# Kernel optimization log

Measured on AMD Instinct MI355X. Metric: run time of the kernel, lower is better.

The kernel has to match this reference:

```python
import jax, jax.numpy as jnp
import numpy as np

HIDDEN = 1024
N_HEADS = 16
HEAD_DIM = HIDDEN // N_HEADS


def setup_inputs() -> dict:
    key = jax.random.key(0)
    ks = jax.random.split(key, 8)
    bs, seq = 8, 1024
    hidden_states = jax.random.normal(ks[0], (bs, seq, HIDDEN), dtype=jnp.float32)
    attention_mask = jnp.zeros((bs, 1, 1, seq), dtype=jnp.float32)
    s = 1.0 / np.sqrt(HIDDEN)
    Wq = jax.random.normal(ks[1], (HIDDEN, HIDDEN), dtype=jnp.float32) * s
    bq = jnp.zeros((HIDDEN,), dtype=jnp.float32)
    Wk = jax.random.normal(ks[2], (HIDDEN, HIDDEN), dtype=jnp.float32) * s
    bk = jnp.zeros((HIDDEN,), dtype=jnp.float32)
    Wv = jax.random.normal(ks[3], (HIDDEN, HIDDEN), dtype=jnp.float32) * s
    bv = jnp.zeros((HIDDEN,), dtype=jnp.float32)
    return {"hidden_states": hidden_states, "attention_mask": attention_mask,
            "Wq": Wq, "bq": bq, "Wk": Wk, "bk": bk, "Wv": Wv, "bv": bv}


def _split_heads(x):
    # [b, s, H] -> [b, h, s, d]
    b, s, _ = x.shape
    return x.reshape(b, s, N_HEADS, HEAD_DIM).transpose(0, 2, 1, 3)


def reference(hidden_states, attention_mask, Wq, bq, Wk, bk, Wv, bv):
    q = _split_heads(hidden_states @ Wq.T + bq)
    k = _split_heads(hidden_states @ Wk.T + bk)
    v = _split_heads(hidden_states @ Wv.T + bv)
    scale = 1.0 / np.sqrt(HEAD_DIM).astype(np.float32)
    scores = jnp.einsum('bhqd,bhkd->bhqk', q, k) * scale + attention_mask
    probs = jax.nn.softmax(scores, axis=-1)  # dropout p=0.0 -> identity
    ctx = jnp.einsum('bhqk,bhkd->bhqd', probs, v)
    b, h, s, d = ctx.shape
    return ctx.transpose(0, 2, 1, 3).reshape(b, s, h * d)
```

## Files before the change

### kernel.cpp

```cpp
#include <hip/hip_runtime.h>
#include <stdint.h>
#include <stddef.h>

#define HIDDEN 1024
#define NHEADS 16
#define HDIM   64
#define BS     8
#define SEQ    1024
#define MTOT   (BS*SEQ)
#define QKV_T  ((size_t)MTOT*HIDDEN)

typedef short    bf16x8 __attribute__((ext_vector_type(8)));
typedef short    bf16x4 __attribute__((ext_vector_type(4)));
typedef float    f32x4  __attribute__((ext_vector_type(4)));
typedef uint16_t u16x4  __attribute__((ext_vector_type(4)));

__device__ __forceinline__ uint16_t f2bf(float f) {
  union { float f; uint32_t u; } c; c.f = f;
  uint32_t u = c.u + 0x7FFFu + ((c.u >> 16) & 1u);
  return (uint16_t)(u >> 16);
}

__device__ __forceinline__ uint32_t cvt_pk_bf16(float lo, float hi) {
  uint32_t r;
  asm("v_cvt_pk_bf16_f32 %0, %1, %2" : "=v"(r) : "v"(lo), "v"(hi));
  return r;
}

__device__ __forceinline__ bf16x4 pack_bf16x4(float a, float b, float c, float d) {
  union { uint2 u; bf16x4 v; } cv;
  cv.u.x = cvt_pk_bf16(a, b);
  cv.u.y = cvt_pk_bf16(c, d);
  return cv.v;
}

__device__ __forceinline__ f32x4 mfma_16x16x16(bf16x4 a, bf16x4 b, f32x4 c) {
#if __has_builtin(__builtin_amdgcn_mfma_f32_16x16x16bf16_1k)
  return __builtin_amdgcn_mfma_f32_16x16x16bf16_1k(a, b, c, 0, 0, 0);
#elif __has_builtin(__builtin_amdgcn_mfma_f32_16x16x16_bf16)
  return __builtin_amdgcn_mfma_f32_16x16x16_bf16(a, b, c, 0, 0, 0);
#else
  f32x4 d;
  asm("v_mfma_f32_16x16x16_bf16 %0, %1, %2, %3"
      : "=&v"(d) : "v"(a), "v"(b), "v"(c));
  return d;
#endif
}

__device__ __forceinline__ float exp2fast(float x) {
#if __has_builtin(__builtin_amdgcn_exp2f)
  return __builtin_amdgcn_exp2f(x);
#else
  return __expf(x * 0.69314718056f);
#endif
}

__device__ __forceinline__ void gload_lds16(const uint16_t* g, uint16_t* lds) {
  __builtin_amdgcn_global_load_lds(
      (const __attribute__((address_space(1))) uint32_t*)g,
      (__attribute__((address_space(3))) uint32_t*)lds, 16, 0, 0);
}

__global__ __launch_bounds__(256) void cvt_kernel(
    const float* __restrict__ hs, const float* __restrict__ wq,
    const float* __restrict__ wk, const float* __restrict__ wv,
    uint16_t* __restrict__ hsb, uint16_t* __restrict__ wcat)
{
  const int i4 = blockIdx.x * 256 + threadIdx.x;
  f32x4 v;
  u16x4 o;
  if (i4 < 2097152) {
    v = *((const f32x4*)hs + i4);
    o[0]=f2bf(v[0]); o[1]=f2bf(v[1]); o[2]=f2bf(v[2]); o[3]=f2bf(v[3]);
    *((u16x4*)hsb + i4) = o;
  } else {
    int j4 = i4 - 2097152;
    int w  = j4 >> 18;
    int r4 = j4 & 262143;
    const float* src = (w == 0) ? wq : ((w == 1) ? wk : wv);
    v = *((const f32x4*)src + r4);
    o[0]=f2bf(v[0]); o[1]=f2bf(v[1]); o[2]=f2bf(v[2]); o[3]=f2bf(v[3]);
    *((u16x4*)wcat + j4) = o;
  }
}

__global__ __launch_bounds__(512, 4) void gemm_qkv(
    const uint16_t* __restrict__ hsb, const uint16_t* __restrict__ wcat,
    const float* __restrict__ bq, const float* __restrict__ bk,
    const float* __restrict__ bv, uint16_t* __restrict__ qbuf,
    uint16_t* __restrict__ kbuf, uint16_t* __restrict__ vtbuf)
{
  __shared__ uint16_t Alds[2][256*32];
  __shared__ uint16_t Blds[2][128*32];

  const int bid = blockIdx.x;
  const int wg  = (bid & 7) * 96 + (bid >> 3);
  const int tm  = wg / 24, tn = wg % 24;
  const int m0  = tm * 256, n0 = tn * 128;
  const int t   = threadIdx.x;
  const int l   = t & 63, w = t >> 6;
  const int wm  = w >> 1, wn = w & 1;
  const int q16 = l & 15;

  f32x4 acc[4][4];
#pragma unroll
  for (int i = 0; i < 4; i++)
#pragma unroll
    for (int j = 0; j < 4; j++) acc[i][j] = (f32x4){0.f,0.f,0.f,0.f};

  const int lrow = l >> 2;
  const int rB   = w * 16 + lrow;
  const int gsw  = (l & 3) ^ ((rB >> 1) & 3);
  const size_t offA0 = (size_t)rB * HIDDEN + gsw * 8;
  const size_t offA1 = (size_t)(128 + rB) * HIDDEN + gsw * 8;
  const size_t offB  = offA0;

  auto STAGE = [&](int buf, int kt) {
    const uint16_t* Ab = hsb  + (size_t)m0 * HIDDEN + kt * 32;
    const uint16_t* Bb = wcat + (size_t)n0 * HIDDEN + kt * 32;
    gload_lds16(Ab + offA0, &Alds[buf][(w * 16) * 32]);
    gload_lds16(Ab + offA1, &Alds[buf][(128 + w * 16) * 32]);
    gload_lds16(Bb + offB,  &Blds[buf][(w * 16) * 32]);
  };

  auto COMPUTE = [&](int buf) {
    bf16x8 af[4], bfr[4];
    const int G = l >> 4;
#pragma unroll
    for (int i = 0; i < 4; i++) {
      int ar = wm * 64 + i * 16 + q16;
      int gs = (G ^ ((ar >> 1) & 3)) & 3;
      af[i] = *(const bf16x8*)&Alds[buf][ar * 32 + gs * 8];
    }
#pragma unroll
    for (int j = 0; j < 4; j++) {
      int br = wn * 64 + j * 16 + q16;
      int gs = (G ^ ((br >> 1) & 3)) & 3;
      bfr[j] = *(const bf16x8*)&Blds[buf][br * 32 + gs * 8];
    }
    __builtin_amdgcn_s_setprio(1);
#pragma unroll
    for (int i = 0; i < 4; i++)
#pragma unroll
      for (int j = 0; j < 4; j++)
        acc[i][j] = __builtin_amdgcn_mfma_f32_16x16x32_bf16(af[i], bfr[j], acc[i][j], 0, 0, 0);
    __builtin_amdgcn_s_setprio(0);
  };

  STAGE(0, 0);
  STAGE(1, 1);
#pragma unroll 1
  for (int kt = 0; kt < 32; ++kt) {
    if (kt < 31) { asm volatile("s_waitcnt vmcnt(3)" ::: "memory"); }
    else         { asm volatile("s_waitcnt vmcnt(0)" ::: "memory"); }
    __builtin_amdgcn_s_barrier();
    __builtin_amdgcn_sched_barrier(0);
    COMPUTE(kt & 1);
    if (kt < 31) {
      __builtin_amdgcn_s_barrier();
      __builtin_amdgcn_sched_barrier(0);
      if (kt < 30) STAGE(kt & 1, kt + 2);
    }
  }

#pragma unroll
  for (int j = 0; j < 4; j++) {
    int n     = n0 + wn * 64 + j * 16 + q16;
    int which = n >> 10, nn = n & 1023;
    const float* bp = (which == 0) ? bq : ((which == 1) ? bk : bv);
    float bias = bp[nn];
    int hh = nn >> 6, dd = nn & 63;
#pragma unroll
    for (int i = 0; i < 4; i++) {
      if (which == 2) {
        int m_  = m0 + wm * 64 + i * 16 + (l >> 4) * 4;
        int b_  = m_ >> 10, s_ = m_ & 1023;
        size_t bhh = (size_t)(b_ * NHEADS + hh);
        uint2 pk;
        pk.x = cvt_pk_bf16(acc[i][j][0] + bias, acc[i][j][1] + bias);
        pk.y = cvt_pk_bf16(acc[i][j][2] + bias, acc[i][j][3] + bias);
        *(uint2*)&vtbuf[(bhh * HDIM + dd) * SEQ + s_] = pk;
      } else {
#pragma unroll
        for (int r = 0; r < 4; r++) {
          int m  = m0 + wm * 64 + i * 16 + (l >> 4) * 4 + r;
          int b_ = m >> 10, s_ = m & 1023;
          float val = acc[i][j][r] + bias;
          size_t bhh = (size_t)(b_ * NHEADS + hh);
          if (which == 0)
            qbuf[(bhh * SEQ + s_) * HDIM + dd] = f2bf(val * 0.18033688011112042f);
          else
            kbuf[(bhh * SEQ + s_) * HDIM + dd] = f2bf(val);
        }
      }
    }
  }
}

__global__ __launch_bounds__(256) void attn_kernel(
    const uint16_t* __restrict__ qb, const uint16_t* __restrict__ kb,
    const uint16_t* __restrict__ vtb, const float* __restrict__ mask,
    float* __restrict__ out)
{
  __shared__ uint16_t Klds[128 * 64];
  __shared__ uint16_t Vlds[64 * 128];
  __shared__ float    mlds[SEQ];

  const int bid = blockIdx.x;
  const int wg  = (bid & 7) * 128 + (bid >> 3);
  const int bh  = wg >> 3;
  const int qt  = wg & 7;
  const int b   = bh >> 4, h = bh & 15;

  const uint16_t* Qg = qb  + (size_t)bh * SEQ * HDIM;
  const uint16_t* Kg = kb  + (size_t)bh * SEQ * HDIM;
  const uint16_t* Vg = vtb + (size_t)bh * HDIM * SEQ;

  const int t = threadIdx.x, l = t & 63, w = t >> 6;
  const int G = l >> 4, q16 = l & 15;

  for (int i = t; i < SEQ; i += 256)
    mlds[i] = mask[b * SEQ + i] * 1.44269504089f;

  const int q0w = qt * 128 + w * 32;
  bf16x8 qf[2][2];
#pragma unroll
  for (int qi = 0; qi < 2; ++qi)
#pragma unroll
    for (int k0 = 0; k0 < 2; ++k0)
      qf[qi][k0] = *(const bf16x8*)(Qg + (size_t)(q0w + qi * 16 + q16) * HDIM + k0 * 32 + G * 8);

  f32x4 O0[4], O1[4];
#pragma unroll
  for (int dt = 0; dt < 4; dt++) { O0[dt] = (f32x4){0,0,0,0}; O1[dt] = (f32x4){0,0,0,0}; }
  float mrow0 = -3e38f, mrow1 = -3e38f, lrow0 = 0.f, lrow1 = 0.f;

  const int srow8 = l >> 3;
  const int gsrcK = (l & 7) ^ srow8;
  const int qsw = q16 & 7;

  auto softmax_q = [&](f32x4 (&scq)[8], bf16x4 (&paq)[8], float& mq, float& lq,
                       f32x4 (&Oq)[4], int ktbase) {
    float pm = -3e38f;
#pragma unroll
    for (int jn = 0; jn < 8; jn++) {
      f32x4 mvj = *(const f32x4*)&mlds[ktbase + jn * 16 + G * 4];
      scq[jn] += mvj;
      pm = fmaxf(pm, fmaxf(fmaxf(scq[jn][0], scq[jn][1]), fmaxf(scq[jn][2], scq[jn][3])));
    }
    pm = fmaxf(pm, __shfl_xor(pm, 16));
    pm = fmaxf(pm, __shfl_xor(pm, 32));
    if (!__all(pm <= mq + 11.0f)) {
      float mn = fmaxf(mq, pm);
      float fs = exp2fast(mq - mn);
      mq = mn; lq *= fs;
#pragma unroll
      for (int dt = 0; dt < 4; dt++) Oq[dt] *= fs;
    }
    float ps = 0.f;
#pragma unroll
    for (int jn = 0; jn < 8; jn++) {
      float p0 = exp2fast(scq[jn][0] - mq);
      float p1 = exp2fast(scq[jn][1] - mq);
      float p2 = exp2fast(scq[jn][2] - mq);
      float p3 = exp2fast(scq[jn][3] - mq);
      ps += (p0 + p1) + (p2 + p3);
      paq[jn] = pack_bf16x4(p0, p1, p2, p3);
    }
    ps += __shfl_xor(ps, 16);
    ps += __shfl_xor(ps, 32);
    lq += ps;
  };

  __syncthreads();

#pragma unroll 1
  for (int kt = 0; kt < 8; ++kt) {
    const int ktbase = kt * 128;
#pragma unroll
    for (int ja = 0; ja < 4; ja++) {
      const int rbK = ja * 32 + w * 8;
      gload_lds16(Kg + (size_t)(ktbase + rbK + srow8) * HDIM + gsrcK * 8,
                  &Klds[rbK * 64]);
      const int rbV = ja * 16 + w * 4;
      const int dV  = rbV + (l >> 4);
      const int gV  = (l & 15) ^ (dV & 7);
      gload_lds16(Vg + (size_t)dV * SEQ + ktbase + gV * 8,
                  &Vlds[rbV * 128]);
    }
    __syncthreads();

    f32x4 sc0[8], sc1[8];
#pragma unroll
    for (int jn = 0; jn < 8; jn++) {
      const int kr  = jn * 16 + q16;
      const int gs0 = (G ^ qsw) & 7;
      const int gs1 = ((4 + G) ^ qsw) & 7;
      bf16x8 kf0 = *(const bf16x8*)&Klds[kr * 64 + gs0 * 8];
      bf16x8 kf1 = *(const bf16x8*)&Klds[kr * 64 + gs1 * 8];
      f32x4 z = (f32x4){0, 0, 0, 0};
      sc0[jn] = __builtin_amdgcn_mfma_f32_16x16x32_bf16(kf0, qf[0][0], z, 0, 0, 0);
      sc0[jn] = __builtin_amdgcn_mfma_f32_16x16x32_bf16(kf1, qf[0][1], sc0[jn], 0, 0, 0);
      sc1[jn] = __builtin_amdgcn_mfma_f32_16x16x32_bf16(kf0, qf[1][0], z, 0, 0, 0);
      sc1[jn] = __builtin_amdgcn_mfma_f32_16x16x32_bf16(kf1, qf[1][1], sc1[jn], 0, 0, 0);
    }

    bf16x4 pa0[8], pa1[8];
    softmax_q(sc0, pa0, mrow0, lrow0, O0, ktbase);
    softmax_q(sc1, pa1, mrow1, lrow1, O1, ktbase);

#pragma unroll
    for (int jn = 0; jn < 8; jn++) {
      const int gq = 2 * jn + (G >> 1);
#pragma unroll
      for (int dt = 0; dt < 4; dt++) {
        const int dr   = dt * 16 + q16;
        const int slot = gq ^ (dr & 7);
        bf16x4 vf = *(const bf16x4*)&Vlds[dr * 128 + slot * 8 + (G & 1) * 4];
        O0[dt] = mfma_16x16x16(vf, pa0[jn], O0[dt]);
        O1[dt] = mfma_16x16x16(vf, pa1[jn], O1[dt]);
      }
    }
    __syncthreads();
  }

  {
    float inv0 = 1.0f / lrow0, inv1 = 1.0f / lrow1;
    int qa = q0w + q16, qb2 = q0w + 16 + q16;
    float* orow0 = out + (size_t)(b * SEQ + qa)  * HIDDEN + h * HDIM;
    float* orow1 = out + (size_t)(b * SEQ + qb2) * HIDDEN + h * HDIM;
#pragma unroll
    for (int dt = 0; dt < 4; dt++) {
      f32x4 a = O0[dt] * inv0;
      f32x4 c = O1[dt] * inv1;
      *(f32x4*)(orow0 + dt * 16 + G * 4) = a;
      *(f32x4*)(orow1 + dt * 16 + G * 4) = c;
    }
  }
}

extern "C" void kernel_launch(void* const* d_in, const int* in_sizes, int n_in,
                              void* d_out, int out_size, void* d_ws, size_t ws_size,
                              hipStream_t stream) {
  const float* hs   = (const float*)d_in[0];
  const float* mask = (const float*)d_in[1];
  const float* Wq   = (const float*)d_in[2];
  const float* bq   = (const float*)d_in[3];
  const float* Wk   = (const float*)d_in[4];
  const float* bk   = (const float*)d_in[5];
  const float* Wv   = (const float*)d_in[6];
  const float* bv   = (const float*)d_in[7];
  float* out = (float*)d_out;

  uint16_t* hsb  = (uint16_t*)d_ws;
  uint16_t* wcat = (uint16_t*)((char*)d_ws + 16777216u);
  uint16_t* qbuf = (uint16_t*)((char*)d_ws + 23068672u);
  uint16_t* kbuf = (uint16_t*)((char*)d_ws + 39845888u);
  uint16_t* vtbf = (uint16_t*)((char*)d_ws + 56623104u);

  cvt_kernel<<<11264, 256, 0, stream>>>(hs, Wq, Wk, Wv, hsb, wcat);
  gemm_qkv<<<768, 512, 0, stream>>>(hsb, wcat, bq, bk, bv, qbuf, kbuf, vtbf);
  attn_kernel<<<1024, 256, 0, stream>>>(qbuf, kbuf, vtbf, mask, out);
}
```

Before: 145.6 us.

## Restructure QKV GEMM into K=64 tiles with four-phase pipelined LDS schedule

The QKV projection GEMM now stages K in 64-wide tiles split into two 32-wide halves across four LDS buffers, doubling prefetch depth. Each iteration runs four compute phases separated by barriers, interleaving global-to-LDS loads for tile kt+2 between phases. B fragments are cached across phases. It also drops the occupancy hint from launch_bounds. The aim is to hide load latency better, at the cost of more LDS use, more barriers, and possibly lower occupancy.

```diff
diff --git a/kernel.cpp b/kernel.cpp
--- a/kernel.cpp
+++ b/kernel.cpp
@@ -84,23 +84,23 @@
   }
 }
 
-__global__ __launch_bounds__(512, 4) void gemm_qkv(
+__global__ __launch_bounds__(512) void gemm_qkv(
     const uint16_t* __restrict__ hsb, const uint16_t* __restrict__ wcat,
     const float* __restrict__ bq, const float* __restrict__ bk,
     const float* __restrict__ bv, uint16_t* __restrict__ qbuf,
     uint16_t* __restrict__ kbuf, uint16_t* __restrict__ vtbuf)
 {
-  __shared__ uint16_t Alds[2][256*32];
-  __shared__ uint16_t Blds[2][128*32];
+  __shared__ uint16_t Ak[4][256*32];
+  __shared__ uint16_t Bk[4][128*32];
 
   const int bid = blockIdx.x;
   const int wg  = (bid & 7) * 96 + (bid >> 3);
   const int tm  = wg / 24, tn = wg % 24;
   const int m0  = tm * 256, n0 = tn * 128;
-  const int t   = threadIdx.x;
-  const int l   = t & 63, w = t >> 6;
+  const int tid = threadIdx.x;
+  const int l   = tid & 63, w = tid >> 6;
   const int wm  = w >> 1, wn = w & 1;
-  const int q16 = l & 15;
+  const int q16 = l & 15, G = l >> 4;
 
   f32x4 acc[4][4];
 #pragma unroll
@@ -109,59 +109,71 @@
     for (int j = 0; j < 4; j++) acc[i][j] = (f32x4){0.f,0.f,0.f,0.f};
 
   const int lrow = l >> 2;
-  const int rB   = w * 16 + lrow;
-  const int gsw  = (l & 3) ^ ((rB >> 1) & 3);
-  const size_t offA0 = (size_t)rB * HIDDEN + gsw * 8;
-  const size_t offA1 = (size_t)(128 + rB) * HIDDEN + gsw * 8;
-  const size_t offB  = offA0;
-
-  auto STAGE = [&](int buf, int kt) {
-    const uint16_t* Ab = hsb  + (size_t)m0 * HIDDEN + kt * 32;
-    const uint16_t* Bb = wcat + (size_t)n0 * HIDDEN + kt * 32;
-    gload_lds16(Ab + offA0, &Alds[buf][(w * 16) * 32]);
-    gload_lds16(Ab + offA1, &Alds[buf][(128 + w * 16) * 32]);
-    gload_lds16(Bb + offB,  &Blds[buf][(w * 16) * 32]);
+  const int gsw  = (l & 3) ^ ((lrow >> 1) & 3);
+
+  auto STAGE = [&](int tile, int kh) {
+    const int sub = (tile & 1) * 2 + kh;
+    const uint16_t* Ab = hsb  + (size_t)m0 * HIDDEN + tile * 64 + kh * 32;
+    const uint16_t* Bb = wcat + (size_t)n0 * HIDDEN + tile * 64 + kh * 32;
+    gload_lds16(Ab + (size_t)(w * 32      + lrow) * HIDDEN + gsw * 8,
+                &Ak[sub][(w * 32) * 32]);
+    gload_lds16(Ab + (size_t)(w * 32 + 16 + lrow) * HIDDEN + gsw * 8,
+                &Ak[sub][(w * 32 + 16) * 32]);
+    gload_lds16(Bb + (size_t)(w * 16      + lrow) * HIDDEN + gsw * 8,
+                &Bk[sub][(w * 16) * 32]);
   };
 
-  auto COMPUTE = [&](int buf) {
-    bf16x8 af[4], bfr[4];
-    const int G = l >> 4;
-#pragma unroll
-    for (int i = 0; i < 4; i++) {
-      int ar = wm * 64 + i * 16 + q16;
+  bf16x8 bcache[4];
+  auto PHASE = [&](int sub, int ih, bool loadB) {
+    bf16x8 af[2];
+#pragma unroll
+    for (int ii = 0; ii < 2; ii++) {
+      int ar = wm * 64 + (ih * 2 + ii) * 16 + q16;
       int gs = (G ^ ((ar >> 1) & 3)) & 3;
-      af[i] = *(const bf16x8*)&Alds[buf][ar * 32 + gs * 8];
-    }
-#pragma unroll
-    for (int j = 0; j < 4; j++) {
-      int br = wn * 64 + j * 16 + q16;
-      int gs = (G ^ ((br >> 1) & 3)) & 3;
-      bfr[j] = *(const bf16x8*)&Blds[buf][br * 32 + gs * 8];
+      af[ii] = *(const bf16x8*)&Ak[sub][ar * 32 + gs * 8];
+    }
+    if (loadB) {
+#pragma unroll
+      for (int j = 0; j < 4; j++) {
+        int br = wn * 64 + j * 16 + q16;
+        int gs = (G ^ ((br >> 1) & 3)) & 3;
+        bcache[j] = *(const bf16x8*)&Bk[sub][br * 32 + gs * 8];
+      }
     }
     __builtin_amdgcn_s_setprio(1);
 #pragma unroll
-    for (int i = 0; i < 4; i++)
+    for (int ii = 0; ii < 2; ii++)
 #pragma unroll
       for (int j = 0; j < 4; j++)
-        acc[i][j] = __builtin_amdgcn_mfma_f32_16x16x32_bf16(af[i], bfr[j], acc[i][j], 0, 0, 0);
+        acc[ih * 2 + ii][j] =
+            __builtin_amdgcn_mfma_f32_16x16x32_bf16(af[ii], bcache[j],
+                                                    acc[ih * 2 + ii][j], 0, 0, 0);
     __builtin_amdgcn_s_setprio(0);
   };
 
-  STAGE(0, 0);
-  STAGE(1, 1);
+#define SBAR() do { __builtin_amdgcn_s_barrier(); \
+                    __builtin_amdgcn_sched_barrier(0); } while (0)
+
+  STAGE(0, 0); STAGE(0, 1); STAGE(1, 0); STAGE(1, 1);
+
 #pragma unroll 1
-  for (int kt = 0; kt < 32; ++kt) {
-    if (kt < 31) { asm volatile("s_waitcnt vmcnt(3)" ::: "memory"); }
+  for (int kt = 0; kt < 16; ++kt) {
+    const int sb = (kt & 1) * 2;
+    if (kt < 15) { asm volatile("s_waitcnt vmcnt(6)" ::: "memory"); }
     else         { asm volatile("s_waitcnt vmcnt(0)" ::: "memory"); }
-    __builtin_amdgcn_s_barrier();
-    __builtin_amdgcn_sched_barrier(0);
-    COMPUTE(kt & 1);
-    if (kt < 31) {
-      __builtin_amdgcn_s_barrier();
-      __builtin_amdgcn_sched_barrier(0);
-      if (kt < 30) STAGE(kt & 1, kt + 2);
-    }
-  }
+    SBAR();
+    PHASE(sb, 0, true);
+    SBAR();
+    PHASE(sb, 1, false);
+    SBAR();
+    if (kt < 14) STAGE(kt + 2, 0);
+    PHASE(sb + 1, 0, true);
+    SBAR();
+    PHASE(sb + 1, 1, false);
+    SBAR();
+    if (kt < 14) STAGE(kt + 2, 1);
+  }
+#undef SBAR
 
 #pragma unroll
   for (int j = 0; j < 4; j++) {
```

Measured after the change: 167.6 us. 15.1% more time.
